# Performance work log

Measured on AMD Instinct MI355X. Metric: run time of the kernel, lower is better.

The kernel has to match this reference:

```python
import jax, jax.numpy as jnp
import numpy as np

N_CODE, PC = 127, 63
LENGTH = N_CODE + PC          # 190
D_MODEL, D_STATE, D_CONV, EXPAND = 512, 16, 4, 2
D_INNER = EXPAND * D_MODEL    # 1024
DT_RANK = (D_MODEL + 15) // 16  # 32
BATCH = 16


def _build_mask(pcm):
    # faithful translation of build_mask(code)
    L = N_CODE + PC
    mask = np.eye(L, dtype=np.float64)
    for r in range(PC):
        idx = np.where(pcm[r] > 0)[0]
        for jj in idx:
            for kk in idx:
                if jj != kk:
                    mask[jj, kk] += 1
                    mask[kk, jj] += 1
                    mask[N_CODE + r, jj] += 1
                    mask[jj, N_CODE + r] += 1
    return mask > 0


def setup_inputs() -> dict:
    rng = np.random.default_rng(0)
    # LDPC-like sparse parity-check matrix, row weight 6
    pcm = np.zeros((PC, N_CODE), np.int32)
    for r in range(PC):
        pcm[r, rng.choice(N_CODE, 6, replace=False)] = 1
    pc_mask = jnp.asarray(_build_mask(pcm))

    def w(shape, fan_in):
        return jnp.asarray((rng.standard_normal(shape) / np.sqrt(fan_in)).astype(np.float32))

    inp = {
        "x": jnp.asarray(rng.standard_normal((BATCH, LENGTH, D_MODEL)).astype(np.float32)),
        "pc_mask": pc_mask,
        # masked resize linears (torch Linear: y = x @ W.T + b)
        "in_resize_w": w((LENGTH, D_MODEL), D_MODEL),
        "in_resize_b": jnp.zeros((LENGTH,), jnp.float32),
        "in_reset_w": w((D_MODEL, LENGTH), LENGTH),
        "in_reset_b": jnp.zeros((D_MODEL,), jnp.float32),
        "out_resize_w": w((LENGTH, D_MODEL), D_MODEL),
        "out_resize_b": jnp.zeros((LENGTH,), jnp.float32),
        "out_reset_w": w((D_MODEL, LENGTH), LENGTH),
        "out_reset_b": jnp.zeros((D_MODEL,), jnp.float32),
        # Mamba block params
        "in_proj_w": w((2 * D_INNER, D_MODEL), D_MODEL),
        "conv_w": w((D_INNER, D_CONV), D_CONV),          # depthwise conv kernels
        "conv_b": jnp.zeros((D_INNER,), jnp.float32),
        "x_proj_w": w((DT_RANK + 2 * D_STATE, D_INNER), D_INNER),
        "dt_proj_w": w((D_INNER, DT_RANK), DT_RANK),
        "dt_proj_b": jnp.full((D_INNER,), -4.6, jnp.float32),  # softplus ~ 0.01
        "A_log": jnp.log(jnp.tile(jnp.arange(1, D_STATE + 1, dtype=jnp.float32), (D_INNER, 1))),
        "D": jnp.ones((D_INNER,), jnp.float32),
        "out_proj_w": w((D_MODEL, D_INNER), D_INNER),
        # LayerNorm over (length, d_model)
        "norm_w": jnp.ones((LENGTH, D_MODEL), jnp.float32),
        "norm_b": jnp.zeros((LENGTH, D_MODEL), jnp.float32),
    }
    return inp


def _forward(x, pc_mask, in_resize_w, in_resize_b, in_reset_w, in_reset_b,
             out_resize_w, out_resize_b, out_reset_w, out_reset_b,
             in_proj_w, conv_w, conv_b, x_proj_w, dt_proj_w, dt_proj_b,
             A_log, D, out_proj_w, norm_w, norm_b):
    dt_rank = dt_proj_w.shape[1]
    d_state = A_log.shape[1]
    d_conv = conv_w.shape[1]

    def mamba(h):
        # h: [B, L, d_model]
        xz = h @ in_proj_w.T                       # [B, L, 2*d_inner]
        xc, z = jnp.split(xz, 2, axis=-1)
        # depthwise causal conv along L
        xt = xc.transpose(0, 2, 1)                 # [B, d_inner, L]
        xt = jax.lax.conv_general_dilated(
            xt, conv_w[:, None, :], (1,), [(d_conv - 1, 0)],
            dimension_numbers=("NCH", "OIH", "NCH"),
            feature_group_count=xt.shape[1])
        xc = jax.nn.silu((xt + conv_b[None, :, None]).transpose(0, 2, 1))  # [B,L,di]
        x_dbl = xc @ x_proj_w.T                    # [B, L, dt_rank+2*ds]
        dt = jax.nn.softplus(x_dbl[..., :dt_rank] @ dt_proj_w.T + dt_proj_b)
        Bm = x_dbl[..., dt_rank:dt_rank + d_state]  # [B, L, ds]
        Cm = x_dbl[..., dt_rank + d_state:]         # [B, L, ds]
        A = -jnp.exp(A_log)                         # [di, ds]
        dA = jnp.exp(dt[..., None] * A)             # [B, L, di, ds]
        dBu = (dt * xc)[..., None] * Bm[:, :, None, :]

        def step(hst, inp):
            a, b = inp
            hst = a * hst + b
            return hst, hst

        h0 = jnp.zeros((dA.shape[0], dA.shape[2], dA.shape[3]), dA.dtype)
        _, hs = jax.lax.scan(step, h0, (dA.transpose(1, 0, 2, 3), dBu.transpose(1, 0, 2, 3)))
        y = jnp.einsum("lbds,bls->bld", hs, Cm) + xc * D
        return (y * jax.nn.silu(z)) @ out_proj_w.T  # [B, L, d_model]

    m = pc_mask.astype(x.dtype)
    h = (x @ in_resize_w.T + in_resize_b) * m[0, 0]
    h = (h @ in_reset_w.T + in_reset_b) * x
    o = mamba(h) + jnp.flip(mamba(jnp.flip(h, 1)), 1)  # bidirectional scan
    o = (o @ out_resize_w.T + out_resize_b) * m        # [B,L,L] * [L,L]
    o = (o @ out_reset_w.T + out_reset_b) * x
    # LayerNorm over last two dims (length, d_model)
    t = jnp.tanh(x)
    mu = jnp.mean(t, axis=(-2, -1), keepdims=True)
    var = jnp.var(t, axis=(-2, -1), keepdims=True)
    out = (t - mu) * jax.lax.rsqrt(var + 1e-5) * norm_w + norm_b
    # original module returns only `out`; `o` is also returned here to keep the
    # (otherwise dead) bidirectional selective-scan path observable.
    return out, o


def reference(x, pc_mask, in_resize_w, in_resize_b, in_reset_w, in_reset_b,
              out_resize_w, out_resize_b, out_reset_w, out_reset_b,
              in_proj_w, conv_w, conv_b, x_proj_w, dt_proj_w, dt_proj_b,
              A_log, D, out_proj_w, norm_w, norm_b):
    return _forward(x, pc_mask, in_resize_w, in_resize_b, in_reset_w, in_reset_b,
                    out_resize_w, out_resize_b, out_reset_w, out_reset_b,
                    in_proj_w, conv_w, conv_b, x_proj_w, dt_proj_w, dt_proj_b,
                    A_log, D, out_proj_w, norm_w, norm_b)
```

## Files before the change

kernel.cpp:

```cpp
#include <hip/hip_runtime.h>
#include <hip/hip_bf16.h>

#define B_    16
#define L_    190
#define LP_   192
#define DM_   512
#define DI_   1024
#define LB_   3040
#define RT_   6080
#define LBDI_ 3112960

typedef __attribute__((ext_vector_type(8))) short bf16x8;
typedef __attribute__((ext_vector_type(4))) float f32x4;
typedef __attribute__((ext_vector_type(4))) unsigned short u16x4;

typedef const __attribute__((address_space(1))) void gvoid;
typedef __attribute__((address_space(3))) void lvoid;
#define LOAD_LDS16(g, l) __builtin_amdgcn_global_load_lds((gvoid*)(g), (lvoid*)(l), 16, 0, 0)

__device__ __forceinline__ float siluf(float v) { return v / (1.f + __expf(-v)); }
__device__ __forceinline__ float softplusf(float v) {
  return v > 0.f ? v + log1pf(__expf(-v)) : log1pf(__expf(v));
}
__device__ __forceinline__ float bf2f(unsigned short u) {
  unsigned int w = (unsigned int)u << 16; return __builtin_bit_cast(float, w);
}

struct Cvt2 { const float* src; __hip_bfloat16* dst; int R, C, Rp, Cp; };
struct CvtPack2 { Cvt2 d[9]; };

__global__ __launch_bounds__(256) void cvt_all3(CvtPack2 p,
    const void* __restrict__ pcm, float* __restrict__ maskf,
    const float* __restrict__ irb, const float* __restrict__ orb,
    float* __restrict__ b_inrs, float* __restrict__ b_outrs)
{
  if (blockIdx.y == 9) {
    __shared__ int votes[3];
    if (threadIdx.x < 3) votes[threadIdx.x] = 0;
    __syncthreads();
    if (threadIdx.x < 48) {
      int idx = threadIdx.x * 191;
      const unsigned char* p8  = (const unsigned char*)pcm;
      const unsigned int*  p32 = (const unsigned int*)pcm;
      if (p8[idx] == 1) atomicAdd(&votes[0], 1);
      unsigned int v = p32[idx];
      if (v == 1u)          atomicAdd(&votes[1], 1);
      if (v == 0x3f800000u) atomicAdd(&votes[2], 1);
    }
    __syncthreads();
    int mode = (votes[0] >= 48) ? 0 : (votes[1] >= 48 ? 1 : (votes[2] >= 48 ? 2 : 0));
    for (int i = blockIdx.x * 256 + threadIdx.x; i < L_ * LP_; i += gridDim.x * 256) {
      int r = i / LP_, c = i % LP_;
      float v = 0.f;
      if (c < L_) {
        int s = r * L_ + c;
        if (mode == 0)      v = ((const unsigned char*)pcm)[s] ? 1.f : 0.f;
        else if (mode == 1) v = ((const int*)pcm)[s] ? 1.f : 0.f;
        else                v = ((const float*)pcm)[s];
      }
      maskf[i] = v;
    }
    if (blockIdx.x == 0 && threadIdx.x < LP_) {
      b_inrs[threadIdx.x]  = (threadIdx.x < L_) ? irb[threadIdx.x] : 0.f;
      b_outrs[threadIdx.x] = (threadIdx.x < L_) ? orb[threadIdx.x] : 0.f;
    }
    return;
  }
  Cvt2 D = p.d[blockIdx.y];
  int n = D.Rp * D.Cp;
  if (D.C == D.Cp) {
    int nsrc = D.R * D.C;
    for (int i4 = (blockIdx.x * 256 + threadIdx.x) * 4; i4 < n; i4 += gridDim.x * 256 * 4) {
      __hip_bfloat16 o[4];
      if (i4 + 3 < nsrc) {
        f32x4 v = *(const f32x4*)(D.src + i4);
        #pragma unroll
        for (int q = 0; q < 4; ++q) o[q] = __float2bfloat16(v[q]);
      } else {
        #pragma unroll
        for (int q = 0; q < 4; ++q) { int i = i4 + q; o[q] = __float2bfloat16(i < nsrc ? D.src[i] : 0.f); }
      }
      *(u16x4*)(D.dst + i4) = *(u16x4*)o;
    }
  } else {
    for (int i = blockIdx.x * 256 + threadIdx.x; i < n; i += gridDim.x * 256) {
      int r = i / D.Cp, c = i - r * D.Cp;
      float v = (r < D.R && c < D.C) ? D.src[(size_t)r * D.C + c] : 0.f;
      D.dst[i] = __float2bfloat16(v);
    }
  }
}

template<int EPI, bool OF32, bool OBF>
__global__ __launch_bounds__(256) void gemm128(
    const __hip_bfloat16* __restrict__ A, int lda, int M,
    const __hip_bfloat16* __restrict__ Bw, int Brows,
    const float* __restrict__ bias, const float* __restrict__ aux,
    float* __restrict__ Cf, __hip_bfloat16* __restrict__ Cb,
    int N, int K)
{
  __shared__ bf16x8 SA[2][512];
  __shared__ bf16x8 SB[2][512];
  const int tid = threadIdx.x;
  const int wave = tid >> 6, lane = tid & 63;
  const int m0 = blockIdx.y * 128, n0 = blockIdx.x * 128;
  const int wm = (wave >> 1) * 64, wn = (wave & 1) * 64;
  const int l15 = lane & 15, lkb = lane >> 4;

  f32x4 acc[4][4] = {};

  auto stage = [&](int bsel, int k0) {
    #pragma unroll
    for (int it = 0; it < 2; ++it) {
      int c = it * 256 + tid;
      int row = c & 127, kb = c >> 7;
      int ar = m0 + row; ar = ar < M ? ar : M - 1;
      const __hip_bfloat16* ga = A + (size_t)ar * lda + (k0 + kb * 8);
      LOAD_LDS16(ga, &SA[bsel][it * 256 + wave * 64]);
      int br = n0 + row; br = br < Brows ? br : Brows - 1;
      const __hip_bfloat16* gb = Bw + (size_t)br * K + (k0 + kb * 8);
      LOAD_LDS16(gb, &SB[bsel][it * 256 + wave * 64]);
    }
  };

  const int nk = K >> 5;
  stage(0, 0);
  __syncthreads();
  int buf = 0;
  for (int kt = 0; kt < nk; ++kt) {
    if (kt + 1 < nk) stage(buf ^ 1, (kt + 1) * 32);
    bf16x8 af[4], bq[4];
    #pragma unroll
    for (int f = 0; f < 4; ++f) {
      af[f] = SA[buf][lkb * 128 + wm + f * 16 + l15];
      bq[f] = SB[buf][lkb * 128 + wn + f * 16 + l15];
    }
    #pragma unroll
    for (int i = 0; i < 4; ++i)
      #pragma unroll
      for (int j = 0; j < 4; ++j)
        acc[i][j] = __builtin_amdgcn_mfma_f32_16x16x32_bf16(af[i], bq[j], acc[i][j], 0, 0, 0);
    __syncthreads();
    buf ^= 1;
  }

  #pragma unroll
  for (int i = 0; i < 4; ++i) {
    int r0 = m0 + wm + i * 16 + (lkb << 2);
    #pragma unroll
    for (int j = 0; j < 4; ++j) {
      int col = n0 + wn + j * 16 + l15;
      if (col >= N) continue;
      #pragma unroll
      for (int r = 0; r < 4; ++r) {
        int row = r0 + r;
        if (row >= M) continue;
        float v = acc[i][j][r];
        if (EPI >= 1) v += bias[col];
        if (EPI == 2) v *= aux[(size_t)row * N + col];
        if (EPI == 3) v = softplusf(v);
        if (EPI == 4) v *= aux[(size_t)(row % L_) * N + col];
        if (OF32) Cf[(size_t)row * N + col] = v;
        if (OBF)  Cb[(size_t)row * N + col] = __float2bfloat16(v);
      }
    }
  }
}

template<int EPI, bool OF32, bool OBF>
__global__ __launch_bounds__(256) void gemm64(
    const __hip_bfloat16* __restrict__ A, int lda, int M,
    const __hip_bfloat16* __restrict__ Bw, int Brows,
    const float* __restrict__ bias, const float* __restrict__ aux,
    float* __restrict__ Cf, __hip_bfloat16* __restrict__ Cb,
    int N, int K)
{
  __shared__ bf16x8 SA[2][256];
  __shared__ bf16x8 SB[2][256];
  const int tid = threadIdx.x;
  const int wave = tid >> 6, lane = tid & 63;
  const int m0 = blockIdx.y * 64, n0 = blockIdx.x * 64;
  const int wm = (wave >> 1) * 32, wn = (wave & 1) * 32;
  const int l15 = lane & 15, lkb = lane >> 4;

  f32x4 acc[2][2] = {};

  auto stage = [&](int bsel, int k0) {
    int row = tid & 63, kb = tid >> 6;
    int ar = m0 + row; ar = ar < M ? ar : M - 1;
    const __hip_bfloat16* ga = A + (size_t)ar * lda + (k0 + kb * 8);
    LOAD_LDS16(ga, &SA[bsel][wave * 64]);
    int br = n0 + row; br = br < Brows ? br : Brows - 1;
    const __hip_bfloat16* gb = Bw + (size_t)br * K + (k0 + kb * 8);
    LOAD_LDS16(gb, &SB[bsel][wave * 64]);
  };

  const int nk = K >> 5;
  stage(0, 0);
  __syncthreads();
  int buf = 0;
  for (int kt = 0; kt < nk; ++kt) {
    if (kt + 1 < nk) stage(buf ^ 1, (kt + 1) * 32);
    bf16x8 af[2], bq[2];
    #pragma unroll
    for (int f = 0; f < 2; ++f) {
      af[f] = SA[buf][lkb * 64 + wm + f * 16 + l15];
      bq[f] = SB[buf][lkb * 64 + wn + f * 16 + l15];
    }
    #pragma unroll
    for (int i = 0; i < 2; ++i)
      #pragma unroll
      for (int j = 0; j < 2; ++j)
        acc[i][j] = __builtin_amdgcn_mfma_f32_16x16x32_bf16(af[i], bq[j], acc[i][j], 0, 0, 0);
    __syncthreads();
    buf ^= 1;
  }

  #pragma unroll
  for (int i = 0; i < 2; ++i) {
    int r0 = m0 + wm + i * 16 + (lkb << 2);
    #pragma unroll
    for (int j = 0; j < 2; ++j) {
      int col = n0 + wn + j * 16 + l15;
      if (col >= N) continue;
      #pragma unroll
      for (int r = 0; r < 4; ++r) {
        int row = r0 + r;
        if (row >= M) continue;
        float v = acc[i][j][r];
        if (EPI >= 1) v += bias[col];
        if (EPI == 2) v *= aux[(size_t)row * N + col];
        if (EPI == 3) v = softplusf(v);
        if (EPI == 4) v *= aux[(size_t)(row % L_) * N + col];
        if (OF32) Cf[(size_t)row * N + col] = v;
        if (OBF)  Cb[(size_t)row * N + col] = __float2bfloat16(v);
      }
    }
  }
}

__global__ __launch_bounds__(256) void gemm64_yz(
    const __hip_bfloat16* __restrict__ Y,
    const __hip_bfloat16* __restrict__ Xz,
    const __hip_bfloat16* __restrict__ Bw,
    __hip_bfloat16* __restrict__ Cb,
    int M, int N, int K)
{
  __shared__ bf16x8 SA[2][256];
  __shared__ bf16x8 SB[2][256];
  const int tid = threadIdx.x;
  const int wave = tid >> 6, lane = tid & 63;
  const int m0 = blockIdx.y * 64, n0 = blockIdx.x * 64;
  const int wm = (wave >> 1) * 32, wn = (wave & 1) * 32;
  const int l15 = lane & 15, lkb = lane >> 4;

  f32x4 acc[2][2] = {};

  auto stage = [&](int bsel, int k0) {
    int row = tid & 63, kb = tid >> 6;
    int ar = m0 + row; ar = ar < M ? ar : M - 1;
    size_t o = (size_t)ar * DI_ + (k0 + kb * 8);
    u16x4 f0 = *(const u16x4*)(Y + o);
    u16x4 f1 = *(const u16x4*)(Y + o + 4);
    u16x4 g0 = *(const u16x4*)(Y + LBDI_ + o);
    u16x4 g1 = *(const u16x4*)(Y + LBDI_ + o + 4);
    size_t zo = (size_t)ar * (2 * DI_) + DI_ + (k0 + kb * 8);
    u16x4 z0 = *(const u16x4*)(Xz + zo);
    u16x4 z1 = *(const u16x4*)(Xz + zo + 4);
    unsigned short av[8];
    #pragma unroll
    for (int q = 0; q < 4; ++q) {
      float v = (bf2f(f0[q]) + bf2f(g0[q])) * siluf(bf2f(z0[q]));
      av[q] = __bfloat16_as_ushort(__float2bfloat16(v));
      float w = (bf2f(f1[q]) + bf2f(g1[q])) * siluf(bf2f(z1[q]));
      av[q + 4] = __bfloat16_as_ushort(__float2bfloat16(w));
    }
    SA[bsel][wave * 64 + row] = *(bf16x8*)av;
    int br = n0 + row; br = br < N ? br : N - 1;
    const __hip_bfloat16* gb = Bw + (size_t)br * K + (k0 + kb * 8);
    LOAD_LDS16(gb, &SB[bsel][wave * 64]);
  };

  const int nk = K >> 5;
  stage(0, 0);
  __syncthreads();
  int buf = 0;
  for (int kt = 0; kt < nk; ++kt) {
    if (kt + 1 < nk) stage(buf ^ 1, (kt + 1) * 32);
    bf16x8 af[2], bq[2];
    #pragma unroll
    for (int f = 0; f < 2; ++f) {
      af[f] = SA[buf][lkb * 64 + wm + f * 16 + l15];
      bq[f] = SB[buf][lkb * 64 + wn + f * 16 + l15];
    }
    #pragma unroll
    for (int i = 0; i < 2; ++i)
      #pragma unroll
      for (int j = 0; j < 2; ++j)
        acc[i][j] = __builtin_amdgcn_mfma_f32_16x16x32_bf16(af[i], bq[j], acc[i][j], 0, 0, 0);
    __syncthreads();
    buf ^= 1;
  }

  #pragma unroll
  for (int i = 0; i < 2; ++i) {
    int r0 = m0 + wm + i * 16 + (lkb << 2);
    #pragma unroll
    for (int j = 0; j < 2; ++j) {
      int col = n0 + wn + j * 16 + l15;
      if (col >= N) continue;
      #pragma unroll
      for (int r = 0; r < 4; ++r) {
        int row = r0 + r;
        if (row >= M) continue;
        Cb[(size_t)row * N + col] = __float2bfloat16(acc[i][j][r]);
      }
    }
  }
}

__global__ __launch_bounds__(256) void conv_silu(
    const __hip_bfloat16* __restrict__ xz, const float* __restrict__ w,
    const float* __restrict__ cb, __hip_bfloat16* __restrict__ xcbf)
{
  int t = blockIdx.x * 256 + threadIdx.x;
  int c4 = (t & (DI_ / 4 - 1)) * 4;
  int bl = t >> 8;
  int l = bl % L_;
  int b = bl / L_;
  const __hip_bfloat16* base = xz + (size_t)b * L_ * (2 * DI_) + c4;
  float xr[7][4];
  #pragma unroll
  for (int j = 0; j < 7; ++j) {
    int gl = l + j - 3;
    if (gl >= 0 && gl < L_) {
      u16x4 v = *(const u16x4*)(base + (size_t)gl * (2 * DI_));
      #pragma unroll
      for (int q = 0; q < 4; ++q) xr[j][q] = bf2f(v[q]);
    } else {
      #pragma unroll
      for (int q = 0; q < 4; ++q) xr[j][q] = 0.f;
    }
  }
  __hip_bfloat16 of[4], ob[4];
  #pragma unroll
  for (int q = 0; q < 4; ++q) {
    int c = c4 + q;
    float w0 = w[c * 4], w1 = w[c * 4 + 1], w2 = w[c * 4 + 2], w3 = w[c * 4 + 3];
    float bias = cb[c];
    float sf = fmaf(w0, xr[0][q], fmaf(w1, xr[1][q], fmaf(w2, xr[2][q], fmaf(w3, xr[3][q], bias))));
    float sb = fmaf(w0, xr[6][q], fmaf(w1, xr[5][q], fmaf(w2, xr[4][q], fmaf(w3, xr[3][q], bias))));
    of[q] = __float2bfloat16(siluf(sf));
    ob[q] = __float2bfloat16(siluf(sb));
  }
  size_t o = (size_t)bl * DI_ + c4;
  *(u16x4*)(xcbf + o)         = *(u16x4*)of;
  *(u16x4*)(xcbf + LBDI_ + o) = *(u16x4*)ob;
}

#define SCT_ 24
#define HS_  17
__global__ __launch_bounds__(256) void scan_v9(
    const __hip_bfloat16* __restrict__ dtb,
    const float* __restrict__ xd,
    const __hip_bfloat16* __restrict__ xc,
    const float* __restrict__ A_log, const float* __restrict__ Dv,
    __hip_bfloat16* __restrict__ y)
{
  __shared__ float sH[256 * HS_];
  __shared__ float sS[256];

  const int tid   = threadIdx.x;
  const int dl    = tid & 31;
  const int chunk = tid >> 5;
  const int dglob = blockIdx.x * 32 + dl;
  const int b     = blockIdx.y;
  const int dir   = blockIdx.z;
  const int rowbase = dir * LB_ + b * L_;
  const unsigned short* xcu = (const unsigned short*)xc;
  const unsigned short* dtu = (const unsigned short*)dtb;
  const float* Arow = A_log + dglob * 16;

  const float A0 = -__expf(Arow[0]);
  bool fast = true;
  #pragma unroll
  for (int s = 1; s < 16; ++s) {
    float As = -__expf(Arow[s]);
    fast = fast && (fabsf(As - (float)(s + 1) * A0) <= 1e-4f * (float)(s + 1));
  }
  const float Dd = Dv[dglob];

  const int cstart = chunk * SCT_;
  const int clen = (cstart + SCT_ <= L_) ? SCT_ : (L_ > cstart ? L_ - cstart : 0);

  auto powers = [&](float e1, float* ep) {
    ep[0] = e1;
    #pragma unroll
    for (int s = 1; s < 16; ++s) ep[s] = ep[(s - 1) >> 1] * ep[s >> 1];
  };

  float h[16];
  #pragma unroll
  for (int s = 0; s < 16; ++s) h[s] = 0.f;
  float dsum = 0.f;
  for (int k = 0; k < clen; ++k) {
    int l   = cstart + k;
    int pos = dir ? (L_ - 1 - l) : l;
    size_t grow = (size_t)(rowbase + pos);
    float dtv = bf2f(dtu[grow * DI_ + dglob]);
    float xcv = bf2f(xcu[grow * DI_ + dglob]);
    float du  = dtv * xcv;
    dsum += dtv;
    const float* brow = xd + grow * 64;
    f32x4 bq0 = *(const f32x4*)(brow + 32);
    f32x4 bq1 = *(const f32x4*)(brow + 36);
    f32x4 bq2 = *(const f32x4*)(brow + 40);
    f32x4 bq3 = *(const f32x4*)(brow + 44);
    float ep[16];
    if (fast) {
      powers(__expf(dtv * A0), ep);
    } else {
      #pragma unroll
      for (int s = 0; s < 16; ++s) ep[s] = __expf(dtv * -__expf(Arow[s]));
    }
    #pragma unroll
    for (int s = 0; s < 16; ++s) {
      float Bv = (s < 4) ? bq0[s & 3] : (s < 8) ? bq1[s & 3] : (s < 12) ? bq2[s & 3] : bq3[s & 3];
      h[s] = fmaf(ep[s], h[s], du * Bv);
    }
  }
  {
    float* hr = sH + tid * HS_;
    #pragma unroll
    for (int s = 0; s < 16; ++s) hr[s] = h[s];
    sS[tid] = dsum;
  }
  __syncthreads();

  float hin[16];
  #pragma unroll
  for (int s = 0; s < 16; ++s) hin[s] = 0.f;
  for (int c = 0; c < chunk; ++c) {
    float S = sS[c * 32 + dl];
    const float* hp = sH + (c * 32 + dl) * HS_;
    float ep[16];
    if (fast) {
      powers(__expf(A0 * S), ep);
    } else {
      #pragma unroll
      for (int s = 0; s < 16; ++s) ep[s] = __expf(-__expf(Arow[s]) * S);
    }
    #pragma unroll
    for (int s = 0; s < 16; ++s)
      hin[s] = fmaf(ep[s], hin[s], hp[s]);
  }

  #pragma unroll
  for (int s = 0; s < 16; ++s) h[s] = hin[s];
  for (int k = 0; k < clen; ++k) {
    int l   = cstart + k;
    int pos = dir ? (L_ - 1 - l) : l;
    size_t grow = (size_t)(rowbase + pos);
    float dtv = bf2f(dtu[grow * DI_ + dglob]);
    float xcv = bf2f(xcu[grow * DI_ + dglob]);
    float du  = dtv * xcv;
    const float* brow = xd + grow * 64;
    f32x4 bq0 = *(const f32x4*)(brow + 32);
    f32x4 bq1 = *(const f32x4*)(brow + 36);
    f32x4 bq2 = *(const f32x4*)(brow + 40);
    f32x4 bq3 = *(const f32x4*)(brow + 44);
    f32x4 cq0 = *(const f32x4*)(brow + 48);
    f32x4 cq1 = *(const f32x4*)(brow + 52);
    f32x4 cq2 = *(const f32x4*)(brow + 56);
    f32x4 cq3 = *(const f32x4*)(brow + 60);
    float ep[16];
    if (fast) {
      powers(__expf(dtv * A0), ep);
    } else {
      #pragma unroll
      for (int s = 0; s < 16; ++s) ep[s] = __expf(dtv * -__expf(Arow[s]));
    }
    float acc = 0.f;
    #pragma unroll
    for (int s = 0; s < 16; ++s) {
      float Bv = (s < 4) ? bq0[s & 3] : (s < 8) ? bq1[s & 3] : (s < 12) ? bq2[s & 3] : bq3[s & 3];
      float Cv = (s < 4) ? cq0[s & 3] : (s < 8) ? cq1[s & 3] : (s < 12) ? cq2[s & 3] : cq3[s & 3];
      h[s] = fmaf(ep[s], h[s], du * Bv);
      acc  = fmaf(h[s], Cv, acc);
    }
    y[grow * DI_ + dglob] = __float2bfloat16(fmaf(xcv, Dd, acc));
  }
}

__global__ __launch_bounds__(256) void ln_partial(const float* __restrict__ x,
                                                  float* __restrict__ partials)
{
  int b = blockIdx.y, ch = blockIdx.x;
  const float* xb = x + (size_t)b * (L_ * DM_);
  int lo = ch * 12160, hi = lo + 12160;
  float s = 0.f, s2 = 0.f;
  for (int i = lo + threadIdx.x; i < hi; i += 256) {
    float t = tanhf(xb[i]);
    s += t; s2 = fmaf(t, t, s2);
  }
  #pragma unroll
  for (int off = 32; off > 0; off >>= 1) { s += __shfl_down(s, off); s2 += __shfl_down(s2, off); }
  __shared__ float rs[4], rs2[4];
  int wid = threadIdx.x >> 6, lane = threadIdx.x & 63;
  if (lane == 0) { rs[wid] = s; rs2[wid] = s2; }
  __syncthreads();
  if (threadIdx.x == 0) {
    partials[(b * 8 + ch) * 2 + 0] = rs[0] + rs[1] + rs[2] + rs[3];
    partials[(b * 8 + ch) * 2 + 1] = rs2[0] + rs2[1] + rs2[2] + rs2[3];
  }
}

__global__ __launch_bounds__(256) void ln_final(const float* __restrict__ x,
    const float* __restrict__ partials,
    const float* __restrict__ nw, const float* __restrict__ nb,
    float* __restrict__ out)
{
  int b = blockIdx.y, ch = blockIdx.x;
  float S = 0.f, S2 = 0.f;
  #pragma unroll
  for (int i = 0; i < 8; ++i) { S += partials[(b * 8 + i) * 2 + 0]; S2 += partials[(b * 8 + i) * 2 + 1]; }
  const float inv = 1.f / (float)(L_ * DM_);
  float mu = S * inv;
  float var = S2 * inv - mu * mu;
  float r = rsqrtf(var + 1e-5f);
  const float* xb = x + (size_t)b * (L_ * DM_);
  float* ob = out + (size_t)b * (L_ * DM_);
  int lo = ch * 12160, hi = lo + 12160;
  for (int i = lo + threadIdx.x; i < hi; i += 256) {
    float t = tanhf(xb[i]);
    ob[i] = fmaf((t - mu) * r, nw[i], nb[i]);
  }
}

extern "C" void kernel_launch(void* const* d_in, const int* in_sizes, int n_in,
                              void* d_out, int out_size, void* d_ws, size_t ws_size,
                              hipStream_t stream)
{
  const float* x            = (const float*)d_in[0];
  const void*  pc_mask      = d_in[1];
  const float* in_resize_w  = (const float*)d_in[2];
  const float* in_resize_b  = (const float*)d_in[3];
  const float* in_reset_w   = (const float*)d_in[4];
  const float* in_reset_b   = (const float*)d_in[5];
  const float* out_resize_w = (const float*)d_in[6];
  const float* out_resize_b = (const float*)d_in[7];
  const float* out_reset_w  = (const float*)d_in[8];
  const float* out_reset_b  = (const float*)d_in[9];
  const float* in_proj_w    = (const float*)d_in[10];
  const float* conv_w       = (const float*)d_in[11];
  const float* conv_b       = (const float*)d_in[12];
  const float* x_proj_w     = (const float*)d_in[13];
  const float* dt_proj_w    = (const float*)d_in[14];
  const float* dt_proj_b    = (const float*)d_in[15];
  const float* A_log        = (const float*)d_in[16];
  const float* Dv           = (const float*)d_in[17];
  const float* out_proj_w   = (const float*)d_in[18];
  const float* norm_w       = (const float*)d_in[19];
  const float* norm_b       = (const float*)d_in[20];

  float* W = (float*)d_ws;
  float* maskf    = W + 0;
  float* b_inrs   = W + 36480;
  float* b_outrs  = W + 36672;
  float* xd       = W + 36864;
  float* partials = W + 425984;
  __hip_bfloat16* BF = (__hip_bfloat16*)(W + 426240);
  __hip_bfloat16* w_inrs  = BF + 0;
  __hip_bfloat16* w_inrt  = BF + 98304;
  __hip_bfloat16* w_inpj  = BF + 196608;
  __hip_bfloat16* w_xpj   = BF + 1245184;
  __hip_bfloat16* w_dtpj  = BF + 1310720;
  __hip_bfloat16* w_outpj = BF + 1343488;
  __hip_bfloat16* w_outrs = BF + 1867776;
  __hip_bfloat16* w_outrt = BF + 1966080;
  __hip_bfloat16* x_bf    = BF + 2064384;
  __hip_bfloat16* h1_bf   = BF + 3620864;
  __hip_bfloat16* h_bf    = BF + 4204544;
  __hip_bfloat16* xz_bf   = BF + 5761024;
  __hip_bfloat16* xc_bf   = BF + 11986944;
  __hip_bfloat16* y_bf    = BF + 18212864;
  __hip_bfloat16* xd_bf   = BF + 24438784;
  __hip_bfloat16* dt_bf   = BF + 24827904;
  __hip_bfloat16* o_pre   = BF + 31053824;
  __hip_bfloat16* o2_bf   = BF + 32610304;

  float* out_ln = (float*)d_out;
  float* out_o  = (float*)d_out + (size_t)LB_ * DM_;

  dim3 blk(256);

  CvtPack2 P;
  P.d[0] = Cvt2{ x,            x_bf,    3040, 512, 3040, 512 };
  P.d[1] = Cvt2{ in_resize_w,  w_inrs,  190, 512, 192, 512 };
  P.d[2] = Cvt2{ in_reset_w,   w_inrt,  512, 190, 512, 192 };
  P.d[3] = Cvt2{ in_proj_w,    w_inpj,  2048, 512, 2048, 512 };
  P.d[4] = Cvt2{ x_proj_w,     w_xpj,   64, 1024, 64, 1024 };
  P.d[5] = Cvt2{ dt_proj_w,    w_dtpj,  1024, 32, 1024, 32 };
  P.d[6] = Cvt2{ out_proj_w,   w_outpj, 512, 1024, 512, 1024 };
  P.d[7] = Cvt2{ out_resize_w, w_outrs, 190, 512, 192, 512 };
  P.d[8] = Cvt2{ out_reset_w,  w_outrt, 512, 190, 512, 192 };
  cvt_all3<<<dim3(256, 10), blk, 0, stream>>>(P, pc_mask, maskf,
      in_resize_b, out_resize_b, b_inrs, b_outrs);

  gemm64<1,false,true><<<dim3(3,48), blk, 0, stream>>>(x_bf, 512, 3040, w_inrs, 192, b_inrs, nullptr, nullptr, h1_bf, LP_, 512);
  gemm64<2,false,true><<<dim3(8,48), blk, 0, stream>>>(h1_bf, LP_, 3040, w_inrt, 512, in_reset_b, x, nullptr, h_bf, 512, LP_);
  gemm128<0,false,true><<<dim3(16,24), blk, 0, stream>>>(h_bf, 512, 3040, w_inpj, 2048, nullptr, nullptr, nullptr, xz_bf, 2048, 512);
  conv_silu<<<dim3(LBDI_/1024), blk, 0, stream>>>(xz_bf, conv_w, conv_b, xc_bf);
  gemm64<0,true,true><<<dim3(1,95), blk, 0, stream>>>(xc_bf, 1024, 6080, w_xpj, 64, nullptr, nullptr, xd, xd_bf, 64, 1024);
  gemm64<3,false,true><<<dim3(16,95), blk, 0, stream>>>(xd_bf, 64, 6080, w_dtpj, 1024, dt_proj_b, nullptr, nullptr, dt_bf, 1024, 32);
  scan_v9<<<dim3(32, 16, 2), blk, 0, stream>>>(dt_bf, xd, xc_bf, A_log, Dv, y_bf);
  gemm64_yz<<<dim3(8,48), blk, 0, stream>>>(y_bf, xz_bf, w_outpj, o_pre, 3040, 512, 1024);
  gemm64<4,false,true><<<dim3(3,48), blk, 0, stream>>>(o_pre, 512, 3040, w_outrs, 192, b_outrs, maskf, nullptr, o2_bf, LP_, 512);
  gemm64<2,true,false><<<dim3(8,48), blk, 0, stream>>>(o2_bf, LP_, 3040, w_outrt, 512, out_reset_b, x, out_o, nullptr, 512, LP_);
  dim3 lgrid(8, B_);
  ln_partial<<<lgrid, blk, 0, stream>>>(x, partials);
  ln_final<<<lgrid, blk, 0, stream>>>(x, partials, norm_w, norm_b, out_ln);
}
```

Before: 274.1 us.

## Fold input resize/reset linears into one weight and fuse small kernels

The two chained input linears are pre-multiplied into a single 512x512 bf16 weight, with a combined bias, so x goes through one GEMM instead of two. That GEMM reads fp32 x directly and converts it while staging to LDS, which removes the separate x-to-bf16 conversion pass. The tanh/LayerNorm partial sums and the combined-bias computation are folded into the conversion kernel, and a new 32-row-tile GEMM is used for the narrow x_proj and out_resize products. Smaller tweaks widen the loads in the yz GEMM and unroll the scan loops. The trade-offs are extra GEMM FLOPs and an extra rounding step from the folded bf16 weight.

```diff
diff --git a/kernel.cpp b/kernel.cpp
--- a/kernel.cpp
+++ b/kernel.cpp
@@ -13,6 +13,7 @@
 typedef __attribute__((ext_vector_type(8))) short bf16x8;
 typedef __attribute__((ext_vector_type(4))) float f32x4;
 typedef __attribute__((ext_vector_type(4))) unsigned short u16x4;
+typedef __attribute__((ext_vector_type(8))) unsigned short u16x8;
 
 typedef const __attribute__((address_space(1))) void gvoid;
 typedef __attribute__((address_space(3))) void lvoid;
@@ -26,15 +27,18 @@
   unsigned int w = (unsigned int)u << 16; return __builtin_bit_cast(float, w);
 }
 
-struct Cvt2 { const float* src; __hip_bfloat16* dst; int R, C, Rp, Cp; };
-struct CvtPack2 { Cvt2 d[9]; };
-
-__global__ __launch_bounds__(256) void cvt_all3(CvtPack2 p,
+struct Cvt2 { const float* src; __hip_bfloat16* dst; int R, C, Rp, Cp, T; };
+struct CvtPack2 { Cvt2 d[8]; };
+
+__global__ __launch_bounds__(256) void cvt_all4(CvtPack2 p,
     const void* __restrict__ pcm, float* __restrict__ maskf,
     const float* __restrict__ irb, const float* __restrict__ orb,
-    float* __restrict__ b_inrs, float* __restrict__ b_outrs)
-{
-  if (blockIdx.y == 9) {
+    float* __restrict__ b_outrs,
+    const float* __restrict__ irw, const float* __restrict__ irtb,
+    float* __restrict__ b_comb,
+    const float* __restrict__ x, float* __restrict__ partials)
+{
+  if (blockIdx.y == 8) {
     __shared__ int votes[3];
     if (threadIdx.x < 3) votes[threadIdx.x] = 0;
     __syncthreads();
@@ -60,15 +64,52 @@
       }
       maskf[i] = v;
     }
-    if (blockIdx.x == 0 && threadIdx.x < LP_) {
-      b_inrs[threadIdx.x]  = (threadIdx.x < L_) ? irb[threadIdx.x] : 0.f;
+    if (blockIdx.x == 0 && threadIdx.x < LP_)
       b_outrs[threadIdx.x] = (threadIdx.x < L_) ? orb[threadIdx.x] : 0.f;
+    return;
+  }
+  if (blockIdx.y == 9) {
+    if (blockIdx.x < 2) {
+      int n = blockIdx.x * 256 + threadIdx.x;
+      const float* wrow = irw + (size_t)n * L_;
+      float s = 0.f;
+      for (int k = 0; k < L_; ++k) s = fmaf(wrow[k], irb[k], s);
+      b_comb[n] = s + irtb[n];
+    }
+    return;
+  }
+  if (blockIdx.y == 10) {
+    if (blockIdx.x < 128) {
+      int bb = blockIdx.x >> 3, ch = blockIdx.x & 7;
+      const float* xb = x + (size_t)bb * (L_ * DM_);
+      int lo = ch * 12160, hi = lo + 12160;
+      float s = 0.f, s2 = 0.f;
+      for (int i = lo + threadIdx.x; i < hi; i += 256) {
+        float t = tanhf(xb[i]);
+        s += t; s2 = fmaf(t, t, s2);
+      }
+      #pragma unroll
+      for (int off = 32; off > 0; off >>= 1) { s += __shfl_down(s, off); s2 += __shfl_down(s2, off); }
+      __shared__ float rs[4], rs2[4];
+      int wid = threadIdx.x >> 6, lane = threadIdx.x & 63;
+      if (lane == 0) { rs[wid] = s; rs2[wid] = s2; }
+      __syncthreads();
+      if (threadIdx.x == 0) {
+        partials[(bb * 8 + ch) * 2 + 0] = rs[0] + rs[1] + rs[2] + rs[3];
+        partials[(bb * 8 + ch) * 2 + 1] = rs2[0] + rs2[1] + rs2[2] + rs2[3];
+      }
     }
     return;
   }
   Cvt2 D = p.d[blockIdx.y];
   int n = D.Rp * D.Cp;
-  if (D.C == D.Cp) {
+  if (D.T) {
+    for (int i = blockIdx.x * 256 + threadIdx.x; i < n; i += gridDim.x * 256) {
+      int r = i / D.Cp, c = i - r * D.Cp;
+      float v = (c < D.C && r < D.R) ? D.src[(size_t)c * D.R + r] : 0.f;
+      D.dst[i] = __float2bfloat16(v);
+    }
+  } else if (D.C == D.Cp) {
     int nsrc = D.R * D.C;
     for (int i4 = (blockIdx.x * 256 + threadIdx.x) * 4; i4 < n; i4 += gridDim.x * 256 * 4) {
       __hip_bfloat16 o[4];
@@ -167,7 +208,7 @@
   }
 }
 
-template<int EPI, bool OF32, bool OBF>
+template<int EPI, bool OF32, bool OBF, bool AF32>
 __global__ __launch_bounds__(256) void gemm64(
     const __hip_bfloat16* __restrict__ A, int lda, int M,
     const __hip_bfloat16* __restrict__ Bw, int Brows,
@@ -188,8 +229,18 @@
   auto stage = [&](int bsel, int k0) {
     int row = tid & 63, kb = tid >> 6;
     int ar = m0 + row; ar = ar < M ? ar : M - 1;
-    const __hip_bfloat16* ga = A + (size_t)ar * lda + (k0 + kb * 8);
-    LOAD_LDS16(ga, &SA[bsel][wave * 64]);
+    if (AF32) {
+      const float* ga = (const float*)A + (size_t)ar * lda + (k0 + kb * 8);
+      f32x4 v0 = *(const f32x4*)ga;
+      f32x4 v1 = *(const f32x4*)(ga + 4);
+      __hip_bfloat16 o[8];
+      #pragma unroll
+      for (int q = 0; q < 4; ++q) { o[q] = __float2bfloat16(v0[q]); o[q + 4] = __float2bfloat16(v1[q]); }
+      SA[bsel][wave * 64 + row] = *(bf16x8*)o;
+    } else {
+      const __hip_bfloat16* ga = A + (size_t)ar * lda + (k0 + kb * 8);
+      LOAD_LDS16(ga, &SA[bsel][wave * 64]);
+    }
     int br = n0 + row; br = br < Brows ? br : Brows - 1;
     const __hip_bfloat16* gb = Bw + (size_t)br * K + (k0 + kb * 8);
     LOAD_LDS16(gb, &SB[bsel][wave * 64]);
@@ -239,6 +290,83 @@
   }
 }
 
+template<int EPI, bool OF32, bool OBF>
+__global__ __launch_bounds__(256) void gemm32(
+    const __hip_bfloat16* __restrict__ A, int lda, int M,
+    const __hip_bfloat16* __restrict__ Bw, int Brows,
+    const float* __restrict__ bias, const float* __restrict__ aux,
+    float* __restrict__ Cf, __hip_bfloat16* __restrict__ Cb,
+    int N, int K)
+{
+  __shared__ bf16x8 SA[2][128];
+  __shared__ bf16x8 SB[2][256];
+  const int tid = threadIdx.x;
+  const int wave = tid >> 6, lane = tid & 63;
+  const int m0 = blockIdx.y * 32, n0 = blockIdx.x * 64;
+  const int wm = (wave >> 1) * 16, wn = (wave & 1) * 32;
+  const int l15 = lane & 15, lkb = lane >> 4;
+
+  f32x4 acc[2] = {};
+
+  auto stage = [&](int bsel, int k0) {
+    if (wave < 2) {
+      int row = tid & 31, kb = tid >> 5;
+      int ar = m0 + row; ar = ar < M ? ar : M - 1;
+      const __hip_bfloat16* ga = A + (size_t)ar * lda + (k0 + kb * 8);
+      LOAD_LDS16(ga, &SA[bsel][wave * 64]);
+    } else {
+      int t2 = tid - 128;
+      {
+        int row = t2 & 63, kb = t2 >> 6;
+        int br = n0 + row; br = br < Brows ? br : Brows - 1;
+        const __hip_bfloat16* gb = Bw + (size_t)br * K + (k0 + kb * 8);
+        LOAD_LDS16(gb, &SB[bsel][(wave - 2) * 64]);
+      }
+      {
+        int s1 = t2 + 128;
+        int row = s1 & 63, kb = s1 >> 6;
+        int br = n0 + row; br = br < Brows ? br : Brows - 1;
+        const __hip_bfloat16* gb = Bw + (size_t)br * K + (k0 + kb * 8);
+        LOAD_LDS16(gb, &SB[bsel][128 + (wave - 2) * 64]);
+      }
+    }
+  };
+
+  const int nk = K >> 5;
+  stage(0, 0);
+  __syncthreads();
+  int buf = 0;
+  for (int kt = 0; kt < nk; ++kt) {
+    if (kt + 1 < nk) stage(buf ^ 1, (kt + 1) * 32);
+    bf16x8 af = SA[buf][lkb * 32 + wm + l15];
+    bf16x8 b0 = SB[buf][lkb * 64 + wn + l15];
+    bf16x8 b1 = SB[buf][lkb * 64 + wn + 16 + l15];
+    acc[0] = __builtin_amdgcn_mfma_f32_16x16x32_bf16(af, b0, acc[0], 0, 0, 0);
+    acc[1] = __builtin_amdgcn_mfma_f32_16x16x32_bf16(af, b1, acc[1], 0, 0, 0);
+    __syncthreads();
+    buf ^= 1;
+  }
+
+  int r0 = m0 + wm + (lkb << 2);
+  #pragma unroll
+  for (int j = 0; j < 2; ++j) {
+    int col = n0 + wn + j * 16 + l15;
+    if (col >= N) continue;
+    #pragma unroll
+    for (int r = 0; r < 4; ++r) {
+      int row = r0 + r;
+      if (row >= M) continue;
+      float v = acc[j][r];
+      if (EPI >= 1) v += bias[col];
+      if (EPI == 2) v *= aux[(size_t)row * N + col];
+      if (EPI == 3) v = softplusf(v);
+      if (EPI == 4) v *= aux[(size_t)(row % L_) * N + col];
+      if (OF32) Cf[(size_t)row * N + col] = v;
+      if (OBF)  Cb[(size_t)row * N + col] = __float2bfloat16(v);
+    }
+  }
+}
+
 __global__ __launch_bounds__(256) void gemm64_yz(
     const __hip_bfloat16* __restrict__ Y,
     const __hip_bfloat16* __restrict__ Xz,
@@ -260,20 +388,14 @@
     int row = tid & 63, kb = tid >> 6;
     int ar = m0 + row; ar = ar < M ? ar : M - 1;
     size_t o = (size_t)ar * DI_ + (k0 + kb * 8);
-    u16x4 f0 = *(const u16x4*)(Y + o);
-    u16x4 f1 = *(const u16x4*)(Y + o + 4);
-    u16x4 g0 = *(const u16x4*)(Y + LBDI_ + o);
-    u16x4 g1 = *(const u16x4*)(Y + LBDI_ + o + 4);
-    size_t zo = (size_t)ar * (2 * DI_) + DI_ + (k0 + kb * 8);
-    u16x4 z0 = *(const u16x4*)(Xz + zo);
-    u16x4 z1 = *(const u16x4*)(Xz + zo + 4);
+    u16x8 f8 = *(const u16x8*)(Y + o);
+    u16x8 g8 = *(const u16x8*)(Y + LBDI_ + o);
+    u16x8 z8 = *(const u16x8*)(Xz + (size_t)ar * (2 * DI_) + DI_ + (k0 + kb * 8));
     unsigned short av[8];
     #pragma unroll
-    for (int q = 0; q < 4; ++q) {
-      float v = (bf2f(f0[q]) + bf2f(g0[q])) * siluf(bf2f(z0[q]));
+    for (int q = 0; q < 8; ++q) {
+      float v = (bf2f(f8[q]) + bf2f(g8[q])) * siluf(bf2f(z8[q]));
       av[q] = __bfloat16_as_ushort(__float2bfloat16(v));
-      float w = (bf2f(f1[q]) + bf2f(g1[q])) * siluf(bf2f(z1[q]));
-      av[q + 4] = __bfloat16_as_ushort(__float2bfloat16(w));
     }
     SA[bsel][wave * 64 + row] = *(bf16x8*)av;
     int br = n0 + row; br = br < N ? br : N - 1;
@@ -360,7 +482,7 @@
 
 #define SCT_ 24
 #define HS_  17
-__global__ __launch_bounds__(256) void scan_v9(
+__global__ __launch_bounds__(256) void scan_v11(
     const __hip_bfloat16* __restrict__ dtb,
     const float* __restrict__ xd,
     const __hip_bfloat16* __restrict__ xc,
@@ -403,6 +525,7 @@
   #pragma unroll
   for (int s = 0; s < 16; ++s) h[s] = 0.f;
   float dsum = 0.f;
+  #pragma unroll 4
   for (int k = 0; k < clen; ++k) {
     int l   = cstart + k;
     int pos = dir ? (L_ - 1 - l) : l;
@@ -457,6 +580,7 @@
 
   #pragma unroll
   for (int s = 0; s < 16; ++s) h[s] = hin[s];
+  #pragma unroll 4
   for (int k = 0; k < clen; ++k) {
     int l   = cstart + k;
     int pos = dir ? (L_ - 1 - l) : l;
@@ -489,29 +613,6 @@
       acc  = fmaf(h[s], Cv, acc);
     }
     y[grow * DI_ + dglob] = __float2bfloat16(fmaf(xcv, Dd, acc));
-  }
-}
-
-__global__ __launch_bounds__(256) void ln_partial(const float* __restrict__ x,
-                                                  float* __restrict__ partials)
-{
-  int b = blockIdx.y, ch = blockIdx.x;
-  const float* xb = x + (size_t)b * (L_ * DM_);
-  int lo = ch * 12160, hi = lo + 12160;
-  float s = 0.f, s2 = 0.f;
-  for (int i = lo + threadIdx.x; i < hi; i += 256) {
-    float t = tanhf(xb[i]);
-    s += t; s2 = fmaf(t, t, s2);
-  }
-  #pragma unroll
-  for (int off = 32; off > 0; off >>= 1) { s += __shfl_down(s, off); s2 += __shfl_down(s2, off); }
-  __shared__ float rs[4], rs2[4];
-  int wid = threadIdx.x >> 6, lane = threadIdx.x & 63;
-  if (lane == 0) { rs[wid] = s; rs2[wid] = s2; }
-  __syncthreads();
-  if (threadIdx.x == 0) {
-    partials[(b * 8 + ch) * 2 + 0] = rs[0] + rs[1] + rs[2] + rs[3];
-    partials[(b * 8 + ch) * 2 + 1] = rs2[0] + rs2[1] + rs2[2] + rs2[3];
   }
 }
 
@@ -565,29 +666,28 @@
 
   float* W = (float*)d_ws;
   float* maskf    = W + 0;
-  float* b_inrs   = W + 36480;
-  float* b_outrs  = W + 36672;
-  float* xd       = W + 36864;
-  float* partials = W + 425984;
-  __hip_bfloat16* BF = (__hip_bfloat16*)(W + 426240);
-  __hip_bfloat16* w_inrs  = BF + 0;
-  __hip_bfloat16* w_inrt  = BF + 98304;
-  __hip_bfloat16* w_inpj  = BF + 196608;
-  __hip_bfloat16* w_xpj   = BF + 1245184;
-  __hip_bfloat16* w_dtpj  = BF + 1310720;
-  __hip_bfloat16* w_outpj = BF + 1343488;
-  __hip_bfloat16* w_outrs = BF + 1867776;
-  __hip_bfloat16* w_outrt = BF + 1966080;
-  __hip_bfloat16* x_bf    = BF + 2064384;
-  __hip_bfloat16* h1_bf   = BF + 3620864;
-  __hip_bfloat16* h_bf    = BF + 4204544;
-  __hip_bfloat16* xz_bf   = BF + 5761024;
-  __hip_bfloat16* xc_bf   = BF + 11986944;
-  __hip_bfloat16* y_bf    = BF + 18212864;
-  __hip_bfloat16* xd_bf   = BF + 24438784;
-  __hip_bfloat16* dt_bf   = BF + 24827904;
-  __hip_bfloat16* o_pre   = BF + 31053824;
-  __hip_bfloat16* o2_bf   = BF + 32610304;
+  float* b_comb   = W + 36480;
+  float* b_outrs  = W + 36992;
+  float* xd       = W + 37184;
+  float* partials = W + 426304;
+  __hip_bfloat16* BF = (__hip_bfloat16*)(W + 426560);
+  __hip_bfloat16* w_inrt  = BF + 0;
+  __hip_bfloat16* w_inpj  = BF + 98304;
+  __hip_bfloat16* w_xpj   = BF + 1146880;
+  __hip_bfloat16* w_dtpj  = BF + 1212416;
+  __hip_bfloat16* w_outpj = BF + 1245184;
+  __hip_bfloat16* w_outrs = BF + 1769472;
+  __hip_bfloat16* w_outrt = BF + 1867776;
+  __hip_bfloat16* w_inrsT = BF + 1966080;
+  __hip_bfloat16* wcomb   = BF + 2064384;
+  __hip_bfloat16* h_bf    = BF + 2326528;
+  __hip_bfloat16* xz_bf   = BF + 3883008;
+  __hip_bfloat16* xc_bf   = BF + 10108928;
+  __hip_bfloat16* y_bf    = BF + 16334848;
+  __hip_bfloat16* xd_bf   = BF + 22560768;
+  __hip_bfloat16* dt_bf   = BF + 22949888;
+  __hip_bfloat16* o_pre   = BF + 29175808;
+  __hip_bfloat16* o2_bf   = BF + 30732288;
 
   float* out_ln = (float*)d_out;
   float* out_o  = (float*)d_out + (size_t)LB_ * DM_;
@@ -595,29 +695,27 @@
   dim3 blk(256);
 
   CvtPack2 P;
-  P.d[0] = Cvt2{ x,            x_bf,    3040, 512, 3040, 512 };
-  P.d[1] = Cvt2{ in_resize_w,  w_inrs,  190, 512, 192, 512 };
-  P.d[2] = Cvt2{ in_reset_w,   w_inrt,  512, 190, 512, 192 };
-  P.d[3] = Cvt2{ in_proj_w,    w_inpj,  2048, 512, 2048, 512 };
-  P.d[4] = Cvt2{ x_proj_w,     w_xpj,   64, 1024, 64, 1024 };
-  P.d[5] = Cvt2{ dt_proj_w,    w_dtpj,  1024, 32, 1024, 32 };
-  P.d[6] = Cvt2{ out_proj_w,   w_outpj, 512, 1024, 512, 1024 };
-  P.d[7] = Cvt2{ out_resize_w, w_outrs, 190, 512, 192, 512 };
-  P.d[8] = Cvt2{ out_reset_w,  w_outrt, 512, 190, 512, 192 };
-  cvt_all3<<<dim3(256, 10), blk, 0, stream>>>(P, pc_mask, maskf,
-      in_resize_b, out_resize_b, b_inrs, b_outrs);
-
-  gemm64<1,false,true><<<dim3(3,48), blk, 0, stream>>>(x_bf, 512, 3040, w_inrs, 192, b_inrs, nullptr, nullptr, h1_bf, LP_, 512);
-  gemm64<2,false,true><<<dim3(8,48), blk, 0, stream>>>(h1_bf, LP_, 3040, w_inrt, 512, in_reset_b, x, nullptr, h_bf, 512, LP_);
+  P.d[0] = Cvt2{ in_reset_w,   w_inrt,  512, 190, 512, 192, 0 };
+  P.d[1] = Cvt2{ in_proj_w,    w_inpj,  2048, 512, 2048, 512, 0 };
+  P.d[2] = Cvt2{ x_proj_w,     w_xpj,   64, 1024, 64, 1024, 0 };
+  P.d[3] = Cvt2{ dt_proj_w,    w_dtpj,  1024, 32, 1024, 32, 0 };
+  P.d[4] = Cvt2{ out_proj_w,   w_outpj, 512, 1024, 512, 1024, 0 };
+  P.d[5] = Cvt2{ out_resize_w, w_outrs, 190, 512, 192, 512, 0 };
+  P.d[6] = Cvt2{ out_reset_w,  w_outrt, 512, 190, 512, 192, 0 };
+  P.d[7] = Cvt2{ in_resize_w,  w_inrsT, 512, 190, 512, 192, 1 };
+  cvt_all4<<<dim3(256, 11), blk, 0, stream>>>(P, pc_mask, maskf,
+      in_resize_b, out_resize_b, b_outrs,
+      in_reset_w, in_reset_b, b_comb, x, partials);
+
+  gemm32<0,false,true><<<dim3(8,16), blk, 0, stream>>>(w_inrt, 192, 512, w_inrsT, 512, nullptr, nullptr, nullptr, wcomb, 512, 192);
+  gemm64<2,false,true,true><<<dim3(8,48), blk, 0, stream>>>((const __hip_bfloat16*)x, 512, 3040, wcomb, 512, b_comb, x, nullptr, h_bf, 512, 512);
   gemm128<0,false,true><<<dim3(16,24), blk, 0, stream>>>(h_bf, 512, 3040, w_inpj, 2048, nullptr, nullptr, nullptr, xz_bf, 2048, 512);
   conv_silu<<<dim3(LBDI_/1024), blk, 0, stream>>>(xz_bf, conv_w, conv_b, xc_bf);
-  gemm64<0,true,true><<<dim3(1,95), blk, 0, stream>>>(xc_bf, 1024, 6080, w_xpj, 64, nullptr, nullptr, xd, xd_bf, 64, 1024);
-  gemm64<3,false,true><<<dim3(16,95), blk, 0, stream>>>(xd_bf, 64, 6080, w_dtpj, 1024, dt_proj_b, nullptr, nullptr, dt_bf, 1024, 32);
-  scan_v9<<<dim3(32, 16, 2), blk, 0, stream>>>(dt_bf, xd, xc_bf, A_log, Dv, y_bf);
+  gemm32<0,true,true><<<dim3(1,190), blk, 0, stream>>>(xc_bf, 1024, 6080, w_xpj, 64, nullptr, nullptr, xd, xd_bf, 64, 1024);
+  gemm64<3,false,true,false><<<dim3(16,95), blk, 0, stream>>>(xd_bf, 64, 6080, w_dtpj, 1024, dt_proj_b, nullptr, nullptr, dt_bf, 1024, 32);
+  scan_v11<<<dim3(32, 16, 2), blk, 0, stream>>>(dt_bf, xd, xc_bf, A_log, Dv, y_bf);
   gemm64_yz<<<dim3(8,48), blk, 0, stream>>>(y_bf, xz_bf, w_outpj, o_pre, 3040, 512, 1024);
-  gemm64<4,false,true><<<dim3(3,48), blk, 0, stream>>>(o_pre, 512, 3040, w_outrs, 192, b_outrs, maskf, nullptr, o2_bf, LP_, 512);
-  gemm64<2,true,false><<<dim3(8,48), blk, 0, stream>>>(o2_bf, LP_, 3040, w_outrt, 512, out_reset_b, x, out_o, nullptr, 512, LP_);
-  dim3 lgrid(8, B_);
-  ln_partial<<<lgrid, blk, 0, stream>>>(x, partials);
-  ln_final<<<lgrid, blk, 0, stream>>>(x, partials, norm_w, norm_b, out_ln);
-}
+  gemm32<4,false,true><<<dim3(3,95), blk, 0, stream>>>(o_pre, 512, 3040, w_outrs, 192, b_outrs, maskf, nullptr, o2_bf, LP_, 512);
+  gemm64<2,true,false,false><<<dim3(8,48), blk, 0, stream>>>(o2_bf, LP_, 3040, w_outrt, 512, out_reset_b, x, out_o, nullptr, 512, LP_);
+  ln_final<<<dim3(8, B_), blk, 0, stream>>>(x, partials, norm_w, norm_b, out_ln);
+}
```

New measurement: 272.4 us. No clear change (-0.6%).
